# Kernel optimization log

Measured on AMD Instinct MI355X. Metric: run time of the kernel, lower is better.

## Reference

```python
import jax, jax.numpy as jnp
import numpy as np

V, E, H, B, S, SRC, NLEV = 50000, 512, 1024, 64, 32, 256, 5


def setup_inputs() -> dict:
    key = jax.random.key(0)
    ks = jax.random.split(key, 16)
    f = lambda k, sh: jax.random.normal(k, sh, dtype=jnp.float32) * 0.02
    z = lambda n: jnp.zeros((n,), jnp.float32)
    return dict(
        inputs=jax.random.randint(ks[0], (NLEV, B, S), 0, V, dtype=jnp.int32),
        input_lens=jax.random.randint(ks[1], (NLEV, B), 2, S + 1, dtype=jnp.int32),
        contexts=jax.random.normal(ks[2], (B, SRC, H), dtype=jnp.float32),
        emb_W=f(ks[3], (V, E)),
        W_ih0=f(ks[4], (4 * H, E)), W_hh0=f(ks[5], (4 * H, H)), b_ih0=z(4 * H), b_hh0=z(4 * H),
        W_ih1=f(ks[6], (4 * H, H)), W_hh1=f(ks[7], (4 * H, H)), b_ih1=z(4 * H), b_hh1=z(4 * H),
        att_in_W=f(ks[8], (H, H)), att_in_b=z(H),
        att_out_W=f(ks[9], (H, 2 * H)), att_out_b=z(H),
        isl_in_W=f(ks[10], (H, E + H)), isl_in_b=z(H),
        isl_out_W=f(ks[11], (H, H + E)), isl_out_b=z(H),
    )


def _lstm_cell(x, h, c, W_ih, W_hh, b_ih, b_hh):
    # torch.nn.LSTMCell gate order: i, f, g, o
    g = x @ W_ih.T + b_ih + h @ W_hh.T + b_hh
    i, f, gg, o = jnp.split(g, 4, axis=-1)
    c2 = jax.nn.sigmoid(f) * c + jax.nn.sigmoid(i) * jnp.tanh(gg)
    h2 = jax.nn.sigmoid(o) * jnp.tanh(c2)
    return h2, c2


def reference(inputs, input_lens, contexts, emb_W,
              W_ih0, W_hh0, b_ih0, b_hh0, W_ih1, W_hh1, b_ih1, b_hh1,
              att_in_W, att_in_b, att_out_W, att_out_b,
              isl_in_W, isl_in_b, isl_out_W, isl_out_b):
    L, Bb, Ss = inputs.shape
    plevels = inputs[:-1]                       # [L-1, B, S] parent levels
    levels = inputs[1:, :, :-1]                 # [L-1, B, S-1] decoded levels
    plens = input_lens[:-1]                     # [L-1, B]
    # mask[idx][1:l-1] = 1 per original code
    pos = jnp.arange(Ss)
    mask = ((pos[None, None, :] >= 1) & (pos[None, None, :] < (plens[..., None] - 1))).astype(contexts.dtype)
    pembs = emb_W[plevels] * mask[..., None]    # [L-1, B, S, E]
    # init_state: pooled masked parent embeddings + pooled encoder context
    pe = pembs.mean(axis=2)                     # [L-1, B, E]
    cm = jnp.broadcast_to(contexts.mean(axis=1)[None], (L - 1, Bb, contexts.shape[-1]))
    h0 = jnp.tanh(jnp.concatenate([pe, cm], -1) @ isl_in_W.T + isl_in_b)   # [L-1, B, H]
    c0 = jnp.tanh(jnp.concatenate([cm, pe], -1) @ isl_out_W.T + isl_out_b)  # [L-1, B, H]
    h0s = jnp.stack([h0, h0], axis=1)           # [L-1, 2, B, H] same init for both layers
    c0s = jnp.stack([c0, c0], axis=1)

    xs_all = emb_W[levels].transpose(0, 2, 1, 3)  # [L-1, T, B, E]

    def run_level(h0_l, c0_l, xs):
        def step(carry, x):
            h, c = carry                         # [2, B, H] each
            h1, c1 = _lstm_cell(x, h[0], c[0], W_ih0, W_hh0, b_ih0, b_hh0)
            h2, c2 = _lstm_cell(h1, h[1], c[1], W_ih1, W_hh1, b_ih1, b_hh1)
            # global (Luong general) attention
            gamma = h2 @ att_in_W.T + att_in_b   # [B, H]
            w = jax.nn.softmax(jnp.einsum('bsh,bh->bs', contexts, gamma), axis=-1)
            ct = jnp.einsum('bs,bsh->bh', w, contexts)
            out = jnp.tanh(jnp.concatenate([ct, h2], -1) @ att_out_W.T + att_out_b)
            return (jnp.stack([h1, h2]), jnp.stack([c1, c2])), out
        (hT, cT), outs = jax.lax.scan(step, (h0_l, c0_l), xs)
        return outs, hT, cT

    outs, hT, cT = jax.vmap(run_level)(h0s, c0s, xs_all)  # outs: [L-1, T, B, H]
    return outs, hT[-1], cT[-1]
```

## Files before the change

kernel.cpp:

```cpp
#include <hip/hip_runtime.h>
#include <math.h>

#define E 512
#define H 1024
#define B 64
#define S 32
#define SRC 256
#define L4 4
#define T 31
#define R 256

typedef unsigned int uint_t;
typedef unsigned short ushort_t;
typedef float f32x4_v __attribute__((ext_vector_type(4)));
typedef short bf16x8_v __attribute__((ext_vector_type(8)));
typedef _Float16 f16x8_v __attribute__((ext_vector_type(8)));

__device__ __forceinline__ void split1(float x, uint_t& h, uint_t& l) {
    uint_t u = __float_as_uint(x);
    h = u >> 16;
    float hf = __uint_as_float(u & 0xFFFF0000u);
    l = __float_as_uint(x - hf) >> 16;
}

__device__ __forceinline__ void split_quad(float4 v, uint2& hi, uint2& lo) {
    uint_t h0, h1, h2, h3, l0, l1, l2, l3;
    split1(v.x, h0, l0); split1(v.y, h1, l1);
    split1(v.z, h2, l2); split1(v.w, h3, l3);
    hi.x = h0 | (h1 << 16); hi.y = h2 | (h3 << 16);
    lo.x = l0 | (l1 << 16); lo.y = l2 | (l3 << 16);
}

__device__ __forceinline__ ushort_t f16of(float x) {
    _Float16 h = (_Float16)x;
    return *(ushort_t*)&h;
}

__device__ __forceinline__ void splitf16(float x, ushort_t& h, ushort_t& l) {
    _Float16 hh = (_Float16)x;
    float hf = (float)hh;
    _Float16 hl = (_Float16)(x - hf);
    h = *(ushort_t*)&hh;
    l = *(ushort_t*)&hl;
}

__device__ __forceinline__ void gl_lds16(const void* g, void* l) {
    __builtin_amdgcn_global_load_lds(
        (const __attribute__((address_space(1))) void*)g,
        (__attribute__((address_space(3))) void*)l, 16, 0, 0);
}

__global__ __launch_bounds__(128) void k_embed(const int* __restrict__ inputs,
                                               const float* __restrict__ embW,
                                               ushort_t* __restrict__ x16) {
    int blk = blockIdx.x;
    int b = blk % B;
    int t = (blk / B) % T;
    int l = blk / (B * T);
    int tok = inputs[(l + 1) * B * S + b * S + t];
    const float4* src = (const float4*)(embW + (long long)tok * E);
    float4 v = src[threadIdx.x];
    uint_t w0 = f16of(v.x) | ((uint_t)f16of(v.y) << 16);
    uint_t w1 = f16of(v.z) | ((uint_t)f16of(v.w) << 16);
    size_t base = ((size_t)t * R + (size_t)l * B + b) * E + threadIdx.x * 4;
    uint2 pk = {w0, w1};
    *(uint2*)(x16 + base) = pk;
}

__global__ __launch_bounds__(128) void k_pe(const int* __restrict__ inputs,
                                            const int* __restrict__ lens,
                                            const float* __restrict__ embW,
                                            ushort_t* __restrict__ phi,
                                            ushort_t* __restrict__ plo) {
    int r = blockIdx.x;
    int l = r >> 6, b = r & 63;
    int plen = lens[l * B + b];
    int send = plen - 1;
    if (send > S) send = S;
    const int* toks = inputs + l * B * S + b * S;
    float4 acc = {0.f, 0.f, 0.f, 0.f};
    for (int s = 1; s < send; ++s) {
        int tok = toks[s];
        float4 v = ((const float4*)(embW + (long long)tok * E))[threadIdx.x];
        acc.x += v.x; acc.y += v.y; acc.z += v.z; acc.w += v.w;
    }
    const float inv = 1.f / 32.f;
    acc.x *= inv; acc.y *= inv; acc.z *= inv; acc.w *= inv;
    uint2 hi, lo; split_quad(acc, hi, lo);
    size_t base = (size_t)r * E + threadIdx.x * 4;
    *(uint2*)(phi + base) = hi;
    *(uint2*)(plo + base) = lo;
}

__global__ __launch_bounds__(256) void k_cm(const float* __restrict__ ctx,
                                            ushort_t* __restrict__ chi,
                                            ushort_t* __restrict__ clo) {
    int b = blockIdx.x;
    int j = threadIdx.x;
    const float4* c4 = (const float4*)(ctx + (size_t)b * SRC * H);
    float4 acc = {0.f, 0.f, 0.f, 0.f};
    for (int s = 0; s < SRC; ++s) {
        float4 v = c4[(size_t)s * (H / 4) + j];
        acc.x += v.x; acc.y += v.y; acc.z += v.z; acc.w += v.w;
    }
    const float inv = 1.f / (float)SRC;
    acc.x *= inv; acc.y *= inv; acc.z *= inv; acc.w *= inv;
    uint2 hi, lo; split_quad(acc, hi, lo);
    size_t base = (size_t)b * H + j * 4;
    *(uint2*)(chi + base) = hi;
    *(uint2*)(clo + base) = lo;
}

__global__ __launch_bounds__(256) void k_wsplit(
    const float* __restrict__ src1, int ld1, int o1, int Ka,
    const float* __restrict__ src2, int ld2, int o2, int Kb,
    int rowmap, ushort_t* __restrict__ dhi, ushort_t* __restrict__ dlo) {
    int n = blockIdx.x;
    int KT = Ka + Kb;
    long long r = rowmap ? ((long long)(n & 3) * H + (n >> 2)) : (long long)n;
    for (int k4 = threadIdx.x; k4 < (KT >> 2); k4 += 256) {
        int k = k4 << 2;
        float4 v = (k < Ka) ? *(const float4*)(src1 + r * ld1 + o1 + k)
                            : *(const float4*)(src2 + r * ld2 + o2 + (k - Ka));
        uint2 hi, lo; split_quad(v, hi, lo);
        size_t base = (size_t)n * KT + k;
        *(uint2*)(dhi + base) = hi;
        *(uint2*)(dlo + base) = lo;
    }
}

__global__ __launch_bounds__(256) void k_wtile(
    const float* __restrict__ src1, int ld1, int o1, int Ka,
    const float* __restrict__ src2, int ld2, int o2, int Kb,
    int rowmap, unsigned char* __restrict__ panel) {
    int cb = blockIdx.x, t = blockIdx.y;
    int KT = Ka + Kb;
    int NT = KT >> 6;
    size_t obase = ((size_t)cb * NT + t) * 16384;
    int k0 = t << 6;
    for (int q = threadIdx.x; q < 512; q += 256) {
        int s = q >> 6, l = q & 63;
        int n = cb * 64 + 8 * s + (l >> 3);
        long long r = rowmap ? ((long long)(n & 3) * H + (n >> 2)) : (long long)n;
        int xorc = ((l & 7) * 16) ^ ((l >> 3) << 4);
        int ke = k0 + (xorc >> 1);
        const float* sp = (ke < Ka) ? (src1 + r * ld1 + o1 + ke)
                                    : (src2 + r * ld2 + o2 + (ke - Ka));
        float4 v01 = *(const float4*)sp;
        float4 v23 = *(const float4*)(sp + 4);
        uint2 h0, l0, h1, l1;
        split_quad(v01, h0, l0);
        split_quad(v23, h1, l1);
        uint4 hi = {h0.x, h0.y, h1.x, h1.y};
        uint4 lo = {l0.x, l0.y, l1.x, l1.y};
        *(uint4*)(panel + obase + s * 1024 + l * 16) = hi;
        *(uint4*)(panel + obase + 8192 + s * 1024 + l * 16) = lo;
    }
}

__global__ __launch_bounds__(256) void k_wtile16(
    const float* __restrict__ src1, int ld1, int Ka,
    const float* __restrict__ src2, int ld2, int Kb,
    int rowmap, unsigned char* __restrict__ panel) {
    int cb = blockIdx.x, t = blockIdx.y;
    int KT = Ka + Kb;
    int NT = KT >> 6;
    size_t obase = ((size_t)cb * NT + t) * 16384;
    int k0 = t << 6;
    for (int q = threadIdx.x; q < 512; q += 256) {
        int s = q >> 6, l = q & 63;
        int n = cb * 64 + 8 * s + (l >> 3);
        long long r = rowmap ? ((long long)(n & 3) * H + (n >> 2)) : (long long)n;
        int xorc = ((l & 7) * 16) ^ ((l >> 3) << 4);
        int ke = k0 + (xorc >> 1);
        const float* sp = (ke < Ka) ? (src1 + r * ld1 + ke)
                                    : (src2 + r * ld2 + (ke - Ka));
        ushort_t hh[8], ll[8];
#pragma unroll
        for (int e = 0; e < 8; ++e) splitf16(sp[e], hh[e], ll[e]);
        uint4 hi = {(uint_t)hh[0] | ((uint_t)hh[1] << 16),
                    (uint_t)hh[2] | ((uint_t)hh[3] << 16),
                    (uint_t)hh[4] | ((uint_t)hh[5] << 16),
                    (uint_t)hh[6] | ((uint_t)hh[7] << 16)};
        uint4 lo = {(uint_t)ll[0] | ((uint_t)ll[1] << 16),
                    (uint_t)ll[2] | ((uint_t)ll[3] << 16),
                    (uint_t)ll[4] | ((uint_t)ll[5] << 16),
                    (uint_t)ll[6] | ((uint_t)ll[7] << 16)};
        *(uint4*)(panel + obase + s * 1024 + l * 16) = hi;
        *(uint4*)(panel + obase + 8192 + s * 1024 + l * 16) = lo;
    }
}

__global__ __launch_bounds__(256) void k_wtile16s(
    const float* __restrict__ src1, int ld1, int Ka,
    const float* __restrict__ src2, int ld2, int Kb,
    unsigned char* __restrict__ panel) {
    int cb = blockIdx.x, t = blockIdx.y;
    int KT = Ka + Kb;
    int NT = KT >> 6;
    size_t obase = ((size_t)cb * NT + t) * 8192;
    int k0 = t << 6;
    for (int q = threadIdx.x; q < 512; q += 256) {
        int s = q >> 6, l = q & 63;
        int n = cb * 64 + 8 * s + (l >> 3);
        long long r = (long long)(n & 3) * H + (n >> 2);
        int xorc = ((l & 7) * 16) ^ ((l >> 3) << 4);
        int ke = k0 + (xorc >> 1);
        const float* sp = (ke < Ka) ? (src1 + r * ld1 + ke)
                                    : (src2 + r * ld2 + (ke - Ka));
        ushort_t hh[8];
#pragma unroll
        for (int e = 0; e < 8; ++e) hh[e] = f16of(sp[e]);
        uint4 hi = {(uint_t)hh[0] | ((uint_t)hh[1] << 16),
                    (uint_t)hh[2] | ((uint_t)hh[3] << 16),
                    (uint_t)hh[4] | ((uint_t)hh[5] << 16),
                    (uint_t)hh[6] | ((uint_t)hh[7] << 16)};
        *(uint4*)(panel + obase + s * 1024 + l * 16) = hi;
    }
}

__global__ __launch_bounds__(256) void k_wtileT(
    const float* __restrict__ src, int ld, int K,
    unsigned char* __restrict__ panel) {
    int cb = blockIdx.x, t = blockIdx.y;
    int NT = K >> 6;
    size_t obase = ((size_t)cb * NT + t) * 16384;
    int k0 = t << 6;
    for (int q = threadIdx.x; q < 512; q += 256) {
        int s = q >> 6, l = q & 63;
        int n = cb * 64 + 8 * s + (l >> 3);
        int xorc = ((l & 7) * 16) ^ ((l >> 3) << 4);
        int ke = k0 + (xorc >> 1);
        float4 v01, v23;
        v01.x = src[(size_t)(ke + 0) * ld + n];
        v01.y = src[(size_t)(ke + 1) * ld + n];
        v01.z = src[(size_t)(ke + 2) * ld + n];
        v01.w = src[(size_t)(ke + 3) * ld + n];
        v23.x = src[(size_t)(ke + 4) * ld + n];
        v23.y = src[(size_t)(ke + 5) * ld + n];
        v23.z = src[(size_t)(ke + 6) * ld + n];
        v23.w = src[(size_t)(ke + 7) * ld + n];
        uint2 h0, l0, h1, l1;
        split_quad(v01, h0, l0);
        split_quad(v23, h1, l1);
        uint4 hi = {h0.x, h0.y, h1.x, h1.y};
        uint4 lo = {l0.x, l0.y, l1.x, l1.y};
        *(uint4*)(panel + obase + s * 1024 + l * 16) = hi;
        *(uint4*)(panel + obase + 8192 + s * 1024 + l * 16) = lo;
    }
}

__global__ __launch_bounds__(256) void k_g2(
    const ushort_t* __restrict__ Ah1, const ushort_t* __restrict__ Al1, int K1,
    const ushort_t* __restrict__ Ah2, const ushort_t* __restrict__ Al2, int K2,
    int a2mod,
    const unsigned char* __restrict__ Bp,
    const float* __restrict__ bias1, const float* __restrict__ bias2,
    int mode, float* __restrict__ C,
    long long strideT, long long strideL, long long strideB, int act,
    ushort_t* __restrict__ ohi, ushort_t* __restrict__ olo) {
    __shared__ __align__(16) unsigned char lds[65536];
    const int tid = threadIdx.x;
    const int lane = tid & 63;
    const int wv = tid >> 6;
    const int wm = wv & 1, wn = wv >> 1;
    const int cblk = blockIdx.x;
    const int mblk = blockIdx.y;
    const int m0 = mblk * 64;
    const int colbase = cblk * 64;
    const int KT = K1 + K2;
    const int NT = KT >> 6;
    const int n1steps = K1 >> 6;
    const size_t pbase = (size_t)cblk * NT * 16384;

    f32x4_v zero = {0.f, 0.f, 0.f, 0.f};
    f32x4_v acc[2][2] = {{zero, zero}, {zero, zero}};
    const int xorc = ((lane & 7) * 16) ^ ((lane >> 3) << 4);
    const int rsub = lane >> 3;

    auto stage = [&](int t, int buf) {
        unsigned char* dstA = lds + buf * 16384;
        unsigned char* dstB = lds + 32768 + buf * 16384;
        {
            const ushort_t *Ph, *Pl; int lda, k0, mod;
            if (t < n1steps) { Ph = Ah1; Pl = Al1; lda = K1; k0 = t << 6; mod = 0; }
            else { Ph = Ah2; Pl = Al2; lda = K2; k0 = (t - n1steps) << 6; mod = a2mod; }
#pragma unroll
            for (int cc = 0; cc < 4; ++cc) {
                int c = wv * 4 + cc;
                int p = c >> 3, s = c & 7;
                int rr = m0 + 8 * s + rsub;
                if (mod) rr &= (mod - 1);
                const ushort_t* plane = p ? Pl : Ph;
                gl_lds16((const unsigned char*)(plane + (size_t)rr * lda + k0) + xorc,
                         dstA + c * 1024);
            }
        }
        {
            const unsigned char* tb = Bp + pbase + (size_t)t * 16384;
#pragma unroll
            for (int cc = 0; cc < 4; ++cc) {
                int c = wv * 4 + cc;
                gl_lds16(tb + c * 1024 + lane * 16, dstB + c * 1024);
            }
        }
    };
    auto compute = [&](int buf) {
        const unsigned char* Ab = lds + buf * 16384;
        const unsigned char* Bb = lds + 32768 + buf * 16384;
#pragma unroll
        for (int kf = 0; kf < 2; ++kf) {
            int colA = (kf * 64 + ((lane >> 4) * 16)) ^ ((lane & 7) << 4);
            bf16x8_v ah[2], al[2], bh[2], bl[2];
#pragma unroll
            for (int i = 0; i < 2; ++i) {
                int rowm = (wm * 2 + i) * 16 + (lane & 15);
                ah[i] = *(const bf16x8_v*)(Ab + rowm * 128 + colA);
                al[i] = *(const bf16x8_v*)(Ab + 8192 + rowm * 128 + colA);
                int rj = (wn * 2 + i) * 16 + (lane & 15);
                bh[i] = *(const bf16x8_v*)(Bb + rj * 128 + colA);
                bl[i] = *(const bf16x8_v*)(Bb + 8192 + rj * 128 + colA);
            }
            __builtin_amdgcn_s_setprio(1);
#pragma unroll
            for (int i = 0; i < 2; ++i)
#pragma unroll
                for (int j = 0; j < 2; ++j) {
                    acc[i][j] = __builtin_amdgcn_mfma_f32_16x16x32_bf16(al[i], bh[j], acc[i][j], 0, 0, 0);
                    acc[i][j] = __builtin_amdgcn_mfma_f32_16x16x32_bf16(ah[i], bl[j], acc[i][j], 0, 0, 0);
                    acc[i][j] = __builtin_amdgcn_mfma_f32_16x16x32_bf16(ah[i], bh[j], acc[i][j], 0, 0, 0);
                }
            __builtin_amdgcn_s_setprio(0);
        }
    };

    stage(0, 0);
    int cur = 0;
    for (int tt = 0; tt < NT; ++tt) {
        if (tt + 1 < NT) {
            stage(tt + 1, cur ^ 1);
            asm volatile("s_waitcnt vmcnt(8)" ::: "memory");
        } else {
            asm volatile("s_waitcnt vmcnt(0)" ::: "memory");
        }
        __builtin_amdgcn_s_barrier();
        __builtin_amdgcn_sched_barrier(0);
        compute(cur);
        __builtin_amdgcn_sched_barrier(0);
        __builtin_amdgcn_s_barrier();
        cur ^= 1;
    }

    const int l16 = lane & 15, g4 = (lane >> 4) * 4;
#pragma unroll
    for (int i = 0; i < 2; ++i) {
#pragma unroll
        for (int r = 0; r < 4; ++r) {
            int m = m0 + wm * 32 + i * 16 + g4 + r;
            long long rowoff = (long long)(m >> 8) * strideT
                             + (long long)((m >> 6) & 3) * strideL
                             + (long long)(m & 63) * strideB;
#pragma unroll
            for (int jj = 0; jj < 2; ++jj) {
                int n = colbase + wn * 32 + jj * 16 + l16;
                float v = acc[i][jj][r];
                if (mode == 0) {
                    if (bias1) v += bias1[n];
                    if (bias2) v += bias2[n];
                    if (act) v = tanhf(v);
                    C[rowoff + n] = v;
                } else {
                    uint_t hu, lu; split1(v, hu, lu);
                    ohi[rowoff + n] = (ushort_t)hu;
                    olo[rowoff + n] = (ushort_t)lu;
                }
            }
        }
    }
}

__global__ __launch_bounds__(256) void k_g2h(
    const ushort_t* __restrict__ A1, int K1,
    const ushort_t* __restrict__ A2, int K2,
    const unsigned char* __restrict__ Bp,
    const float* __restrict__ bias1,
    float* __restrict__ C,
    long long strideT, long long strideL, long long strideB) {
    __shared__ __align__(16) unsigned char lds[49152];
    const int tid = threadIdx.x;
    const int lane = tid & 63;
    const int wv = tid >> 6;
    const int wm = wv & 1, wn = wv >> 1;
    const int cblk = blockIdx.x;
    const int m0 = blockIdx.y * 64;
    const int colbase = cblk * 64;
    const int KT = K1 + K2;
    const int NT = KT >> 6;
    const int n1steps = K1 >> 6;
    const size_t pbase = (size_t)cblk * NT * 16384;

    f32x4_v zero = {0.f, 0.f, 0.f, 0.f};
    f32x4_v acc[2][2] = {{zero, zero}, {zero, zero}};
    const int xorc = ((lane & 7) * 16) ^ ((lane >> 3) << 4);
    const int rsub = lane >> 3;

    auto stage = [&](int t, int buf) {
        unsigned char* base = lds + buf * 24576;
        const ushort_t* Ap; int lda, k0;
        if (t < n1steps) { Ap = A1; lda = K1; k0 = t << 6; }
        else             { Ap = A2; lda = K2; k0 = (t - n1steps) << 6; }
        const unsigned char* tb = Bp + pbase + (size_t)t * 16384;
#pragma unroll
        for (int cc = 0; cc < 6; ++cc) {
            int c = wv * 6 + cc;
            if (c < 8) {
                int rr = m0 + 8 * c + rsub;
                gl_lds16((const unsigned char*)(Ap + (size_t)rr * lda + k0) + xorc,
                         base + c * 1024);
            } else {
                gl_lds16(tb + (c - 8) * 1024 + lane * 16, base + c * 1024);
            }
        }
    };
    auto compute = [&](int buf) {
        const unsigned char* Ab = lds + buf * 24576;
        const unsigned char* Bb = Ab + 8192;
#pragma unroll
        for (int kf = 0; kf < 2; ++kf) {
            int colA = (kf * 64 + ((lane >> 4) * 16)) ^ ((lane & 7) << 4);
            f16x8_v a[2], bh[2], bl[2];
#pragma unroll
            for (int i = 0; i < 2; ++i) {
                int rowm = (wm * 2 + i) * 16 + (lane & 15);
                a[i] = *(const f16x8_v*)(Ab + rowm * 128 + colA);
                int rj = (wn * 2 + i) * 16 + (lane & 15);
                bh[i] = *(const f16x8_v*)(Bb + rj * 128 + colA);
                bl[i] = *(const f16x8_v*)(Bb + 8192 + rj * 128 + colA);
            }
            __builtin_amdgcn_s_setprio(1);
#pragma unroll
            for (int i = 0; i < 2; ++i)
#pragma unroll
                for (int j = 0; j < 2; ++j) {
                    acc[i][j] = __builtin_amdgcn_mfma_f32_16x16x32_f16(a[i], bl[j], acc[i][j], 0, 0, 0);
                    acc[i][j] = __builtin_amdgcn_mfma_f32_16x16x32_f16(a[i], bh[j], acc[i][j], 0, 0, 0);
                }
            __builtin_amdgcn_s_setprio(0);
        }
    };

    stage(0, 0);
    int cur = 0;
    for (int tt = 0; tt < NT; ++tt) {
        if (tt + 1 < NT) {
            stage(tt + 1, cur ^ 1);
            asm volatile("s_waitcnt vmcnt(6)" ::: "memory");
        } else {
            asm volatile("s_waitcnt vmcnt(0)" ::: "memory");
        }
        __builtin_amdgcn_s_barrier();
        __builtin_amdgcn_sched_barrier(0);
        compute(cur);
        __builtin_amdgcn_sched_barrier(0);
        __builtin_amdgcn_s_barrier();
        cur ^= 1;
    }

    const int l16 = lane & 15, g4 = (lane >> 4) * 4;
#pragma unroll
    for (int i = 0; i < 2; ++i) {
#pragma unroll
        for (int r = 0; r < 4; ++r) {
            int m = m0 + wm * 32 + i * 16 + g4 + r;
            long long rowoff = (long long)(m >> 8) * strideT
                             + (long long)((m >> 6) & 3) * strideL
                             + (long long)(m & 63) * strideB;
#pragma unroll
            for (int jj = 0; jj < 2; ++jj) {
                int n = colbase + wn * 32 + jj * 16 + l16;
                C[rowoff + n] = tanhf(acc[i][jj][r] + bias1[n]);
            }
        }
    }
}

struct GateJob {
    const ushort_t *A1, *A2;
    const unsigned char* Bp;
    const float *bias1, *bias2;
    float *cbuf, *hf;
    ushort_t *h16;
    ushort_t *hhi, *hlo;
    int K1, K2;
};

__global__ __launch_bounds__(256) void k_gatepair(GateJob j0, GateJob j1) {
    __shared__ __align__(16) unsigned char lds[32768];
    const bool sec = blockIdx.y >= 4;
    const ushort_t* A1v = sec ? j1.A1 : j0.A1;
    const ushort_t* A2v = sec ? j1.A2 : j0.A2;
    const unsigned char* Bp = sec ? j1.Bp : j0.Bp;
    const float* bias1  = sec ? j1.bias1 : j0.bias1;
    const float* bias2  = sec ? j1.bias2 : j0.bias2;
    float* cbuf         = sec ? j1.cbuf : j0.cbuf;
    float* hf           = sec ? j1.hf   : j0.hf;
    ushort_t* h16       = sec ? j1.h16  : j0.h16;
    ushort_t* hhi       = sec ? j1.hhi  : j0.hhi;
    ushort_t* hlo       = sec ? j1.hlo  : j0.hlo;
    const int K1        = sec ? j1.K1   : j0.K1;
    const int K2        = sec ? j1.K2   : j0.K2;

    const int tid = threadIdx.x;
    const int lane = tid & 63;
    const int wv = tid >> 6;
    const int wm = wv & 1, wn = wv >> 1;
    const int mblk = blockIdx.y & 3;
    const int cblk = blockIdx.x;
    const int m0 = mblk * 64;
    const int KT = K1 + K2;
    const int NT = KT >> 6;
    const int n1steps = K1 >> 6;
    const size_t pbase = (size_t)cblk * NT * 8192;

    f32x4_v zero = {0.f, 0.f, 0.f, 0.f};
    f32x4_v acc[2][2] = {{zero, zero}, {zero, zero}};
    const int xorc = ((lane & 7) * 16) ^ ((lane >> 3) << 4);
    const int rsub = lane >> 3;

    auto stage = [&](int t, int buf) {
        unsigned char* base = lds + buf * 16384;
        const ushort_t* Ap; int lda, k0;
        if (t < n1steps) { Ap = A1v; lda = K1; k0 = t << 6; }
        else             { Ap = A2v; lda = K2; k0 = (t - n1steps) << 6; }
        const unsigned char* tb = Bp + pbase + (size_t)t * 8192;
#pragma unroll
        for (int cc = 0; cc < 4; ++cc) {
            int c = wv * 4 + cc;
            if (c < 8) {
                int rr = m0 + 8 * c + rsub;
                gl_lds16((const unsigned char*)(Ap + (size_t)rr * lda + k0) + xorc,
                         base + c * 1024);
            } else {
                gl_lds16(tb + (c - 8) * 1024 + lane * 16, base + c * 1024);
            }
        }
    };
    auto compute = [&](int buf) {
        const unsigned char* Ab = lds + buf * 16384;
        const unsigned char* Bb = Ab + 8192;
#pragma unroll
        for (int kf = 0; kf < 2; ++kf) {
            int colA = (kf * 64 + ((lane >> 4) * 16)) ^ ((lane & 7) << 4);
            f16x8_v a[2], bv[2];
#pragma unroll
            for (int i = 0; i < 2; ++i) {
                int rowm = (wm * 2 + i) * 16 + (lane & 15);
                a[i] = *(const f16x8_v*)(Ab + rowm * 128 + colA);
                int rj = (wn * 2 + i) * 16 + (lane & 15);
                bv[i] = *(const f16x8_v*)(Bb + rj * 128 + colA);
            }
            __builtin_amdgcn_s_setprio(1);
#pragma unroll
            for (int i = 0; i < 2; ++i)
#pragma unroll
                for (int j = 0; j < 2; ++j)
                    acc[i][j] = __builtin_amdgcn_mfma_f32_16x16x32_f16(a[i], bv[j], acc[i][j], 0, 0, 0);
            __builtin_amdgcn_s_setprio(0);
        }
    };

    stage(0, 0);
    int cur = 0;
    for (int tt = 0; tt < NT; ++tt) {
        if (tt + 1 < NT) {
            stage(tt + 1, cur ^ 1);
            asm volatile("s_waitcnt vmcnt(4)" ::: "memory");
        } else {
            asm volatile("s_waitcnt vmcnt(0)" ::: "memory");
        }
        __builtin_amdgcn_s_barrier();
        __builtin_amdgcn_sched_barrier(0);
        compute(cur);
        __builtin_amdgcn_sched_barrier(0);
        __builtin_amdgcn_s_barrier();
        cur ^= 1;
    }

    float* gtile = (float*)lds;
    const int l16 = lane & 15, g4 = (lane >> 4) * 4;
#pragma unroll
    for (int i = 0; i < 2; ++i)
#pragma unroll
        for (int jj = 0; jj < 2; ++jj)
#pragma unroll
            for (int r = 0; r < 4; ++r)
                gtile[(wm * 32 + i * 16 + g4 + r) * 68 + wn * 32 + jj * 16 + l16] = acc[i][jj][r];
    __syncthreads();

    int m = tid >> 2;
    int hcb = (tid & 3) * 4;
    int nh0 = cblk * 16;
#pragma unroll
    for (int e = 0; e < 4; ++e) {
        int hc = hcb + e;
        float gv[4];
#pragma unroll
        for (int q = 0; q < 4; ++q) {
            int bidx = q * H + nh0 + hc;
            gv[q] = gtile[m * 68 + hc * 4 + q] + bias1[bidx] + bias2[bidx];
        }
        size_t idx = (size_t)(m0 + m) * H + nh0 + hc;
        float cp = cbuf[idx];
        float si = 1.f / (1.f + __expf(-gv[0]));
        float sf = 1.f / (1.f + __expf(-gv[1]));
        float so = 1.f / (1.f + __expf(-gv[3]));
        float c = sf * cp + si * tanhf(gv[2]);
        float hn = so * tanhf(c);
        cbuf[idx] = c;
        hf[idx] = hn;
        h16[idx] = f16of(hn);
        if (hhi) {
            uint_t hu, lu; split1(hn, hu, lu);
            hhi[idx] = (ushort_t)hu;
            hlo[idx] = (ushort_t)lu;
        }
    }
}

__global__ __launch_bounds__(256) void k_smfma(
    const ushort_t* __restrict__ h1h, const ushort_t* __restrict__ h1l,
    const ushort_t* __restrict__ cwh, const ushort_t* __restrict__ cwl,
    float* __restrict__ scores) {
    __shared__ __align__(16) unsigned char lds[65536];
    const int tid = threadIdx.x;
    const int lane = tid & 63;
    const int wv = tid >> 6;
    const int wm = wv & 1, wn = wv >> 1;
    const int b = blockIdx.z;
    const int m0 = blockIdx.y * 64;
    const int colbase = blockIdx.x * 64;
    const int NT = 16;

    f32x4_v zero = {0.f, 0.f, 0.f, 0.f};
    f32x4_v acc[2][2] = {{zero, zero}, {zero, zero}};
    const int xorc = ((lane & 7) * 16) ^ ((lane >> 3) << 4);
    const int rsub = lane >> 3;

    auto stage = [&](int t, int buf) {
        unsigned char* dstA = lds + buf * 16384;
        unsigned char* dstB = lds + 32768 + buf * 16384;
        int k0 = t << 6;
#pragma unroll
        for (int cc = 0; cc < 4; ++cc) {
            int c = wv * 4 + cc;
            int p = c >> 3, s = c & 7;
            int rr = m0 + 8 * s + rsub;
            int tt = rr >> 2; if (tt > 30) tt = 30;
            size_t row = (size_t)tt * R + (rr & 3) * 64 + b;
            const ushort_t* plane = p ? h1l : h1h;
            gl_lds16((const unsigned char*)(plane + row * H + k0) + xorc,
                     dstA + c * 1024);
        }
#pragma unroll
        for (int cc = 0; cc < 4; ++cc) {
            int c = wv * 4 + cc;
            int p = c >> 3, s = c & 7;
            int rr = colbase + 8 * s + rsub;
            const ushort_t* plane = p ? cwl : cwh;
            gl_lds16((const unsigned char*)(plane + ((size_t)b * SRC + rr) * H + k0) + xorc,
                     dstB + c * 1024);
        }
    };
    auto compute = [&](int buf) {
        const unsigned char* Ab = lds + buf * 16384;
        const unsigned char* Bb = lds + 32768 + buf * 16384;
#pragma unroll
        for (int kf = 0; kf < 2; ++kf) {
            int colA = (kf * 64 + ((lane >> 4) * 16)) ^ ((lane & 7) << 4);
            bf16x8_v ah[2], al[2], bh[2], bl[2];
#pragma unroll
            for (int i = 0; i < 2; ++i) {
                int rowm = (wm * 2 + i) * 16 + (lane & 15);
                ah[i] = *(const bf16x8_v*)(Ab + rowm * 128 + colA);
                al[i] = *(const bf16x8_v*)(Ab + 8192 + rowm * 128 + colA);
                int rj = (wn * 2 + i) * 16 + (lane & 15);
                bh[i] = *(const bf16x8_v*)(Bb + rj * 128 + colA);
                bl[i] = *(const bf16x8_v*)(Bb + 8192 + rj * 128 + colA);
            }
            __builtin_amdgcn_s_setprio(1);
#pragma unroll
            for (int i = 0; i < 2; ++i)
#pragma unroll
                for (int j = 0; j < 2; ++j) {
                    acc[i][j] = __builtin_amdgcn_mfma_f32_16x16x32_bf16(al[i], bh[j], acc[i][j], 0, 0, 0);
                    acc[i][j] = __builtin_amdgcn_mfma_f32_16x16x32_bf16(ah[i], bl[j], acc[i][j], 0, 0, 0);
                    acc[i][j] = __builtin_amdgcn_mfma_f32_16x16x32_bf16(ah[i], bh[j], acc[i][j], 0, 0, 0);
                }
            __builtin_amdgcn_s_setprio(0);
        }
    };

    stage(0, 0);
    int cur = 0;
    for (int tt = 0; tt < NT; ++tt) {
        if (tt + 1 < NT) {
            stage(tt + 1, cur ^ 1);
            asm volatile("s_waitcnt vmcnt(8)" ::: "memory");
        } else {
            asm volatile("s_waitcnt vmcnt(0)" ::: "memory");
        }
        __builtin_amdgcn_s_barrier();
        __builtin_amdgcn_sched_barrier(0);
        compute(cur);
        __builtin_amdgcn_sched_barrier(0);
        __builtin_amdgcn_s_barrier();
        cur ^= 1;
    }

    const int l16 = lane & 15, g4 = (lane >> 4) * 4;
#pragma unroll
    for (int i = 0; i < 2; ++i) {
#pragma unroll
        for (int jj = 0; jj < 2; ++jj) {
#pragma unroll
            for (int r = 0; r < 4; ++r) {
                int m = m0 + wm * 32 + i * 16 + g4 + r;
                int t = m >> 2;
                if (t < 31) {
                    size_t row = (size_t)t * R + (m & 3) * 64 + b;
                    int n = colbase + wn * 32 + jj * 16 + l16;
                    scores[row * SRC + n] = acc[i][jj][r];
                }
            }
        }
    }
}

__global__ __launch_bounds__(256) void k_smax(const float* __restrict__ scores,
                                              const float* __restrict__ cb,
                                              float* __restrict__ w) {
    int t = blockIdx.x, b = blockIdx.y;
    int l = threadIdx.x >> 6, lane = threadIdx.x & 63;
    size_t row = (size_t)t * R + l * 64 + b;
    const float* sr = scores + row * SRC;
    const float* cbb = cb + b * SRC;
    float v0 = sr[lane] + cbb[lane];
    float v1 = sr[lane + 64] + cbb[lane + 64];
    float v2 = sr[lane + 128] + cbb[lane + 128];
    float v3 = sr[lane + 192] + cbb[lane + 192];
    float m = fmaxf(fmaxf(v0, v1), fmaxf(v2, v3));
#pragma unroll
    for (int off = 32; off >= 1; off >>= 1) m = fmaxf(m, __shfl_xor(m, off));
    float e0 = expf(v0 - m), e1 = expf(v1 - m), e2 = expf(v2 - m), e3 = expf(v3 - m);
    float sum = e0 + e1 + e2 + e3;
#pragma unroll
    for (int off = 32; off >= 1; off >>= 1) sum += __shfl_xor(sum, off);
    float inv = 1.f / sum;
    float* wr = w + row * SRC;
    wr[lane] = e0 * inv;
    wr[lane + 64] = e1 * inv;
    wr[lane + 128] = e2 * inv;
    wr[lane + 192] = e3 * inv;
}

__global__ __launch_bounds__(512) void k_ct_all(const float* __restrict__ ctx,
                                                const float* __restrict__ w,
                                                ushort_t* __restrict__ ct16) {
    __shared__ float ws[32][260];
    const int b = blockIdx.x, tc = blockIdx.y;
    const int tid = threadIdx.x;
    for (int q = tid; q < 32 * 64; q += 512) {
        int r = q >> 6, c4 = q & 63;
        int t = tc * 8 + (r >> 2);
        float4 v = {0.f, 0.f, 0.f, 0.f};
        if (t < 31)
            v = *(const float4*)(w + ((size_t)t * R + (r & 3) * 64 + b) * SRC + c4 * 4);
        *(float4*)&ws[r][c4 * 4] = v;
    }
    __syncthreads();

    float2 acc[32];
#pragma unroll
    for (int r = 0; r < 32; ++r) acc[r] = make_float2(0.f, 0.f);
    const float2* base = (const float2*)(ctx + (size_t)b * SRC * H) + tid;
    for (int s = 0; s < SRC; s += 4) {
        float2 c0 = base[(size_t)s * (H / 2)];
        float2 c1 = base[(size_t)(s + 1) * (H / 2)];
        float2 c2 = base[(size_t)(s + 2) * (H / 2)];
        float2 c3 = base[(size_t)(s + 3) * (H / 2)];
#pragma unroll
        for (int r = 0; r < 32; ++r) {
            float4 wv = *(const float4*)&ws[r][s];
            acc[r].x += wv.x * c0.x + wv.y * c1.x + wv.z * c2.x + wv.w * c3.x;
            acc[r].y += wv.x * c0.y + wv.y * c1.y + wv.z * c2.y + wv.w * c3.y;
        }
    }
#pragma unroll
    for (int r = 0; r < 32; ++r) {
        int t = tc * 8 + (r >> 2);
        if (t < 31) {
            size_t obase = ((size_t)t * R + (r & 3) * 64 + b) * H + tid * 2;
            uint_t pk = f16of(acc[r].x) | ((uint_t)f16of(acc[r].y) << 16);
            *(uint_t*)(ct16 + obase) = pk;
        }
    }
}

__global__ __launch_bounds__(256) void k_init_split(const float* __restrict__ h0f,
                                                    const float* __restrict__ c0f,
                                                    float* __restrict__ h1f,
                                                    float* __restrict__ c1f,
                                                    ushort_t* __restrict__ h0_16,
                                                    ushort_t* __restrict__ h1i_16) {
    int idx = blockIdx.x * 256 + threadIdx.x;
    float h = h0f[idx], c = c0f[idx];
    h1f[idx] = h; c1f[idx] = c;
    ushort_t hv = f16of(h);
    h0_16[idx] = hv;
    h1i_16[idx] = hv;
}

__global__ __launch_bounds__(256) void k_cb(const float* __restrict__ ctx,
                                            const float* __restrict__ bvec,
                                            float* __restrict__ cb) {
    int b = blockIdx.x, ch = blockIdx.y;
    int wave = threadIdx.x >> 6, lane = threadIdx.x & 63;
    for (int i = 0; i < 16; ++i) {
        int s = ch * 64 + wave * 16 + i;
        const float* cs = ctx + ((size_t)b * SRC + s) * H;
        float a = 0.f;
#pragma unroll
        for (int j = 0; j < 4; ++j) {
            float4 cv = *(const float4*)(cs + lane * 4 + j * 256);
            float4 bv = *(const float4*)(bvec + lane * 4 + j * 256);
            a += cv.x * bv.x + cv.y * bv.y + cv.z * bv.z + cv.w * bv.w;
        }
#pragma unroll
        for (int off = 32; off >= 1; off >>= 1) a += __shfl_xor(a, off);
        if (lane == 0) cb[b * SRC + s] = a;
    }
}

extern "C" void kernel_launch(void* const* d_in, const int* in_sizes, int n_in,
                              void* d_out, int out_size, void* d_ws, size_t ws_size,
                              hipStream_t stream) {
    const int*   inputs     = (const int*)d_in[0];
    const int*   input_lens = (const int*)d_in[1];
    const float* contexts   = (const float*)d_in[2];
    const float* emb_W      = (const float*)d_in[3];
    const float* W_ih0      = (const float*)d_in[4];
    const float* W_hh0      = (const float*)d_in[5];
    const float* b_ih0      = (const float*)d_in[6];
    const float* b_hh0      = (const float*)d_in[7];
    const float* W_ih1      = (const float*)d_in[8];
    const float* W_hh1      = (const float*)d_in[9];
    const float* b_ih1      = (const float*)d_in[10];
    const float* b_hh1      = (const float*)d_in[11];
    const float* att_in_W   = (const float*)d_in[12];
    const float* att_in_b   = (const float*)d_in[13];
    const float* att_out_W  = (const float*)d_in[14];
    const float* att_out_b  = (const float*)d_in[15];
    const float* isl_in_W   = (const float*)d_in[16];
    const float* isl_in_b   = (const float*)d_in[17];
    const float* isl_out_W  = (const float*)d_in[18];
    const float* isl_out_b  = (const float*)d_in[19];

    float* out = (float*)d_out;

    char* p = (char*)d_ws;
    auto alloc = [&](size_t bytes) { char* r = p; p += (bytes + 255) & ~(size_t)255; return r; };
    ushort_t* xs16 = (ushort_t*)alloc((size_t)T * R * E * 2);
    ushort_t* h016[2];
    h016[0] = (ushort_t*)alloc((size_t)R * H * 2);
    h016[1] = (ushort_t*)alloc((size_t)R * H * 2);
    ushort_t* h1i16 = (ushort_t*)alloc((size_t)R * H * 2);
    ushort_t* h116all = (ushort_t*)alloc((size_t)T * R * H * 2);
    ushort_t* h1hall = (ushort_t*)alloc((size_t)T * R * H * 2);
    ushort_t* h1lall = (ushort_t*)alloc((size_t)T * R * H * 2);
    ushort_t* pehi = (ushort_t*)alloc((size_t)R * E * 2);
    ushort_t* pelo = (ushort_t*)alloc((size_t)R * E * 2);
    ushort_t* cmhi = (ushort_t*)alloc((size_t)B * H * 2);
    ushort_t* cmlo = (ushort_t*)alloc((size_t)B * H * 2);
    unsigned char* wg0p = (unsigned char*)alloc((size_t)64 * 24 * 8192);
    unsigned char* wg1p = (unsigned char*)alloc((size_t)64 * 32 * 8192);
    unsigned char* wgTp = (unsigned char*)alloc((size_t)16 * 16 * 16384);
    unsigned char* wotp = (unsigned char*)alloc((size_t)16 * 32 * 16384);
    unsigned char* wiip = (unsigned char*)alloc((size_t)16 * 24 * 16384);
    unsigned char* wiop = (unsigned char*)alloc((size_t)16 * 24 * 16384);
    ushort_t* cxh = (ushort_t*)alloc((size_t)B * SRC * H * 2);
    ushort_t* cxl = (ushort_t*)alloc((size_t)B * SRC * H * 2);
    ushort_t* cwh = (ushort_t*)alloc((size_t)B * SRC * H * 2);
    ushort_t* cwl = (ushort_t*)alloc((size_t)B * SRC * H * 2);
    float* cbv = (float*)alloc((size_t)B * SRC * 4);
    float* h0f = (float*)alloc((size_t)R * H * 4);
    float* h1f = (float*)alloc((size_t)R * H * 4);
    float* c0f = (float*)alloc((size_t)R * H * 4);
    float* c1f = (float*)alloc((size_t)R * H * 4);
    float* scores = (float*)cxh;
    float* wbuf   = scores + (size_t)T * R * SRC;
    ushort_t* ct16 = (ushort_t*)(wbuf + (size_t)T * R * SRC);

    k_embed<<<L4 * T * B, 128, 0, stream>>>(inputs, emb_W, xs16);
    k_pe<<<R, 128, 0, stream>>>(inputs, input_lens, emb_W, pehi, pelo);
    k_cm<<<B, 256, 0, stream>>>(contexts, cmhi, cmlo);
    k_wtile16s<<<dim3(64, 24), 256, 0, stream>>>(W_ih0, 512, 512, W_hh0, 1024, 1024, wg0p);
    k_wtile16s<<<dim3(64, 32), 256, 0, stream>>>(W_ih1, 1024, 1024, W_hh1, 1024, 1024, wg1p);
    k_wtile16<<<dim3(16, 32), 256, 0, stream>>>(att_out_W, 2048, 2048, nullptr, 0, 0, 0, wotp);
    k_wtileT<<<dim3(16, 16), 256, 0, stream>>>(att_in_W, 1024, 1024, wgTp);
    k_wtile<<<dim3(16, 24), 256, 0, stream>>>(isl_in_W, 1536, 0, 1536, nullptr, 0, 0, 0, 0, wiip);
    k_wtile<<<dim3(16, 24), 256, 0, stream>>>(isl_out_W, 1536, 1024, 512, isl_out_W, 1536, 0, 1024, 0, wiop);
    k_wsplit<<<B * SRC, 256, 0, stream>>>(contexts, 1024, 0, 1024, nullptr, 0, 0, 0, 0, cxh, cxl);

    k_g2<<<dim3(16, 4), 256, 0, stream>>>(pehi, pelo, 512, cmhi, cmlo, 1024, 64,
                                          wiip, isl_in_b, nullptr, 0,
                                          h0f, 0, 64LL * H, (long long)H, 1,
                                          nullptr, nullptr);
    k_g2<<<dim3(16, 4), 256, 0, stream>>>(pehi, pelo, 512, cmhi, cmlo, 1024, 64,
                                          wiop, isl_out_b, nullptr, 0,
                                          c0f, 0, 64LL * H, (long long)H, 1,
                                          nullptr, nullptr);
    k_init_split<<<R * H / 256, 256, 0, stream>>>(h0f, c0f, h1f, c1f, h016[0], h1i16);

    k_g2<<<dim3(16, 256), 256, 0, stream>>>(cxh, cxl, 1024,
                                            nullptr, nullptr, 0, 0,
                                            wgTp, nullptr, nullptr, 2,
                                            nullptr, (long long)SRC * H, 64LL * H, (long long)H, 0,
                                            cwh, cwl);
    k_cb<<<dim3(B, 4), 256, 0, stream>>>(contexts, att_in_b, cbv);

    int cur = 0;
    for (int L = 0; L <= T; ++L) {
        bool has0 = (L < T), has1 = (L > 0);
        GateJob g0 = {}, g1 = {};
        if (has0) {
            g0.A1 = xs16 + (size_t)L * R * E;
            g0.A2 = h016[cur];
            g0.Bp = wg0p;
            g0.bias1 = b_ih0;  g0.bias2 = b_hh0;
            g0.cbuf = c0f;  g0.hf = h0f;
            g0.h16 = h016[cur ^ 1];
            g0.hhi = nullptr;  g0.hlo = nullptr;
            g0.K1 = E;  g0.K2 = H;
        }
        if (has1) {
            g1.A1 = h016[cur];
            g1.A2 = (L == 1) ? h1i16 : h116all + (size_t)(L - 2) * R * H;
            g1.Bp = wg1p;
            g1.bias1 = b_ih1;  g1.bias2 = b_hh1;
            g1.cbuf = c1f;  g1.hf = h1f;
            g1.h16 = h116all + (size_t)(L - 1) * R * H;
            g1.hhi = h1hall + (size_t)(L - 1) * R * H;
            g1.hlo = h1lall + (size_t)(L - 1) * R * H;
            g1.K1 = H;  g1.K2 = H;
        }
        if (has0 && has1)
            k_gatepair<<<dim3(64, 8), 256, 0, stream>>>(g0, g1);
        else if (has0)
            k_gatepair<<<dim3(64, 4), 256, 0, stream>>>(g0, g0);
        else
            k_gatepair<<<dim3(64, 4), 256, 0, stream>>>(g1, g1);
        if (has0) cur ^= 1;
    }

    k_smfma<<<dim3(4, 2, B), 256, 0, stream>>>(h1hall, h1lall, cwh, cwl, scores);
    k_smax<<<dim3(T, B), 256, 0, stream>>>(scores, cbv, wbuf);
    k_ct_all<<<dim3(B, 4), 512, 0, stream>>>(contexts, wbuf, ct16);
    k_g2h<<<dim3(16, 124), 256, 0, stream>>>(ct16, 1024, h116all, 1024,
                                             wotp, att_out_b,
                                             out, (long long)B * H,
                                             (long long)T * B * H, (long long)H);

    size_t OUTS = (size_t)L4 * T * B * H;
    size_t seg = (size_t)B * H;
    hipMemcpyAsync(out + OUTS,           h0f + 192 * H, seg * 4, hipMemcpyDeviceToDevice, stream);
    hipMemcpyAsync(out + OUTS + seg,     h1f + 192 * H, seg * 4, hipMemcpyDeviceToDevice, stream);
    hipMemcpyAsync(out + OUTS + 2 * seg, c0f + 192 * H, seg * 4, hipMemcpyDeviceToDevice, stream);
    hipMemcpyAsync(out + OUTS + 3 * seg, c1f + 192 * H, seg * 4, hipMemcpyDeviceToDevice, stream);
}
```

Measured before the change: 1.256 ms.

## Compute attention gamma per step instead of projecting contexts; deepen gate pipeline

The old path projected every context row through att_in_W (a 16K-row GEMM) and added a separate bias-score kernel. The new path applies att_in_W to the decoded h2 states instead, producing gamma in hi/lo split form, and scores gamma against the raw split contexts. This removes the large context projection, the bias dot-product kernel and the hi/lo split writes inside the recurrent gate kernel. Separately, the gate kernel's K-loop goes from double buffering to a 4-stage LDS pipeline with 64KB of shared memory, which may reduce occupancy.

```diff
diff --git a/kernel.cpp b/kernel.cpp
--- a/kernel.cpp
+++ b/kernel.cpp
@@ -219,37 +219,6 @@
     }
 }
 
-__global__ __launch_bounds__(256) void k_wtileT(
-    const float* __restrict__ src, int ld, int K,
-    unsigned char* __restrict__ panel) {
-    int cb = blockIdx.x, t = blockIdx.y;
-    int NT = K >> 6;
-    size_t obase = ((size_t)cb * NT + t) * 16384;
-    int k0 = t << 6;
-    for (int q = threadIdx.x; q < 512; q += 256) {
-        int s = q >> 6, l = q & 63;
-        int n = cb * 64 + 8 * s + (l >> 3);
-        int xorc = ((l & 7) * 16) ^ ((l >> 3) << 4);
-        int ke = k0 + (xorc >> 1);
-        float4 v01, v23;
-        v01.x = src[(size_t)(ke + 0) * ld + n];
-        v01.y = src[(size_t)(ke + 1) * ld + n];
-        v01.z = src[(size_t)(ke + 2) * ld + n];
-        v01.w = src[(size_t)(ke + 3) * ld + n];
-        v23.x = src[(size_t)(ke + 4) * ld + n];
-        v23.y = src[(size_t)(ke + 5) * ld + n];
-        v23.z = src[(size_t)(ke + 6) * ld + n];
-        v23.w = src[(size_t)(ke + 7) * ld + n];
-        uint2 h0, l0, h1, l1;
-        split_quad(v01, h0, l0);
-        split_quad(v23, h1, l1);
-        uint4 hi = {h0.x, h0.y, h1.x, h1.y};
-        uint4 lo = {l0.x, l0.y, l1.x, l1.y};
-        *(uint4*)(panel + obase + s * 1024 + l * 16) = hi;
-        *(uint4*)(panel + obase + 8192 + s * 1024 + l * 16) = lo;
-    }
-}
-
 __global__ __launch_bounds__(256) void k_g2(
     const ushort_t* __restrict__ Ah1, const ushort_t* __restrict__ Al1, int K1,
     const ushort_t* __restrict__ Ah2, const ushort_t* __restrict__ Al2, int K2,
@@ -384,8 +353,9 @@
     const ushort_t* __restrict__ A2, int K2,
     const unsigned char* __restrict__ Bp,
     const float* __restrict__ bias1,
-    float* __restrict__ C,
-    long long strideT, long long strideL, long long strideB) {
+    int mode, float* __restrict__ C,
+    long long strideT, long long strideL, long long strideB,
+    ushort_t* __restrict__ ohi, ushort_t* __restrict__ olo) {
     __shared__ __align__(16) unsigned char lds[49152];
     const int tid = threadIdx.x;
     const int lane = tid & 63;
@@ -478,7 +448,14 @@
 #pragma unroll
             for (int jj = 0; jj < 2; ++jj) {
                 int n = colbase + wn * 32 + jj * 16 + l16;
-                C[rowoff + n] = tanhf(acc[i][jj][r] + bias1[n]);
+                float v = acc[i][jj][r] + bias1[n];
+                if (mode == 0) {
+                    C[rowoff + n] = tanhf(v);
+                } else {
+                    uint_t hu, lu; split1(v, hu, lu);
+                    ohi[rowoff + n] = (ushort_t)hu;
+                    olo[rowoff + n] = (ushort_t)lu;
+                }
             }
         }
     }
@@ -490,12 +467,11 @@
     const float *bias1, *bias2;
     float *cbuf, *hf;
     ushort_t *h16;
-    ushort_t *hhi, *hlo;
     int K1, K2;
 };
 
 __global__ __launch_bounds__(256) void k_gatepair(GateJob j0, GateJob j1) {
-    __shared__ __align__(16) unsigned char lds[32768];
+    __shared__ __align__(16) unsigned char lds[65536];
     const bool sec = blockIdx.y >= 4;
     const ushort_t* A1v = sec ? j1.A1 : j0.A1;
     const ushort_t* A2v = sec ? j1.A2 : j0.A2;
@@ -505,8 +481,6 @@
     float* cbuf         = sec ? j1.cbuf : j0.cbuf;
     float* hf           = sec ? j1.hf   : j0.hf;
     ushort_t* h16       = sec ? j1.h16  : j0.h16;
-    ushort_t* hhi       = sec ? j1.hhi  : j0.hhi;
-    ushort_t* hlo       = sec ? j1.hlo  : j0.hlo;
     const int K1        = sec ? j1.K1   : j0.K1;
     const int K2        = sec ? j1.K2   : j0.K2;
 
@@ -570,20 +544,24 @@
     };
 
     stage(0, 0);
-    int cur = 0;
+    stage(1, 1);
+    stage(2, 2);
     for (int tt = 0; tt < NT; ++tt) {
-        if (tt + 1 < NT) {
-            stage(tt + 1, cur ^ 1);
+        if (tt + 3 < NT) {
+            stage(tt + 3, (tt + 3) & 3);
+            asm volatile("s_waitcnt vmcnt(12)" ::: "memory");
+        } else if (tt + 2 < NT) {
+            asm volatile("s_waitcnt vmcnt(8)" ::: "memory");
+        } else if (tt + 1 < NT) {
             asm volatile("s_waitcnt vmcnt(4)" ::: "memory");
         } else {
             asm volatile("s_waitcnt vmcnt(0)" ::: "memory");
         }
         __builtin_amdgcn_s_barrier();
         __builtin_amdgcn_sched_barrier(0);
-        compute(cur);
+        compute(tt & 3);
         __builtin_amdgcn_sched_barrier(0);
         __builtin_amdgcn_s_barrier();
-        cur ^= 1;
     }
 
     float* gtile = (float*)lds;
@@ -619,17 +597,12 @@
         cbuf[idx] = c;
         hf[idx] = hn;
         h16[idx] = f16of(hn);
-        if (hhi) {
-            uint_t hu, lu; split1(hn, hu, lu);
-            hhi[idx] = (ushort_t)hu;
-            hlo[idx] = (ushort_t)lu;
-        }
     }
 }
 
 __global__ __launch_bounds__(256) void k_smfma(
-    const ushort_t* __restrict__ h1h, const ushort_t* __restrict__ h1l,
-    const ushort_t* __restrict__ cwh, const ushort_t* __restrict__ cwl,
+    const ushort_t* __restrict__ gah, const ushort_t* __restrict__ gal,
+    const ushort_t* __restrict__ cxh, const ushort_t* __restrict__ cxl,
     float* __restrict__ scores) {
     __shared__ __align__(16) unsigned char lds[65536];
     const int tid = threadIdx.x;
@@ -657,7 +630,7 @@
             int rr = m0 + 8 * s + rsub;
             int tt = rr >> 2; if (tt > 30) tt = 30;
             size_t row = (size_t)tt * R + (rr & 3) * 64 + b;
-            const ushort_t* plane = p ? h1l : h1h;
+            const ushort_t* plane = p ? gal : gah;
             gl_lds16((const unsigned char*)(plane + row * H + k0) + xorc,
                      dstA + c * 1024);
         }
@@ -666,7 +639,7 @@
             int c = wv * 4 + cc;
             int p = c >> 3, s = c & 7;
             int rr = colbase + 8 * s + rsub;
-            const ushort_t* plane = p ? cwl : cwh;
+            const ushort_t* plane = p ? cxl : cxh;
             gl_lds16((const unsigned char*)(plane + ((size_t)b * SRC + rr) * H + k0) + xorc,
                      dstB + c * 1024);
         }
@@ -737,17 +710,15 @@
 }
 
 __global__ __launch_bounds__(256) void k_smax(const float* __restrict__ scores,
-                                              const float* __restrict__ cb,
                                               float* __restrict__ w) {
     int t = blockIdx.x, b = blockIdx.y;
     int l = threadIdx.x >> 6, lane = threadIdx.x & 63;
     size_t row = (size_t)t * R + l * 64 + b;
     const float* sr = scores + row * SRC;
-    const float* cbb = cb + b * SRC;
-    float v0 = sr[lane] + cbb[lane];
-    float v1 = sr[lane + 64] + cbb[lane + 64];
-    float v2 = sr[lane + 128] + cbb[lane + 128];
-    float v3 = sr[lane + 192] + cbb[lane + 192];
+    float v0 = sr[lane];
+    float v1 = sr[lane + 64];
+    float v2 = sr[lane + 128];
+    float v3 = sr[lane + 192];
     float m = fmaxf(fmaxf(v0, v1), fmaxf(v2, v3));
 #pragma unroll
     for (int off = 32; off >= 1; off >>= 1) m = fmaxf(m, __shfl_xor(m, off));
@@ -818,27 +789,6 @@
     ushort_t hv = f16of(h);
     h0_16[idx] = hv;
     h1i_16[idx] = hv;
-}
-
-__global__ __launch_bounds__(256) void k_cb(const float* __restrict__ ctx,
-                                            const float* __restrict__ bvec,
-                                            float* __restrict__ cb) {
-    int b = blockIdx.x, ch = blockIdx.y;
-    int wave = threadIdx.x >> 6, lane = threadIdx.x & 63;
-    for (int i = 0; i < 16; ++i) {
-        int s = ch * 64 + wave * 16 + i;
-        const float* cs = ctx + ((size_t)b * SRC + s) * H;
-        float a = 0.f;
-#pragma unroll
-        for (int j = 0; j < 4; ++j) {
-            float4 cv = *(const float4*)(cs + lane * 4 + j * 256);
-            float4 bv = *(const float4*)(bvec + lane * 4 + j * 256);
-            a += cv.x * bv.x + cv.y * bv.y + cv.z * bv.z + cv.w * bv.w;
-        }
-#pragma unroll
-        for (int off = 32; off >= 1; off >>= 1) a += __shfl_xor(a, off);
-        if (lane == 0) cb[b * SRC + s] = a;
-    }
 }
 
 extern "C" void kernel_launch(void* const* d_in, const int* in_sizes, int n_in,
@@ -875,38 +825,35 @@
     h016[1] = (ushort_t*)alloc((size_t)R * H * 2);
     ushort_t* h1i16 = (ushort_t*)alloc((size_t)R * H * 2);
     ushort_t* h116all = (ushort_t*)alloc((size_t)T * R * H * 2);
-    ushort_t* h1hall = (ushort_t*)alloc((size_t)T * R * H * 2);
-    ushort_t* h1lall = (ushort_t*)alloc((size_t)T * R * H * 2);
+    ushort_t* gamh = (ushort_t*)alloc((size_t)T * R * H * 2);
+    ushort_t* gaml = (ushort_t*)alloc((size_t)T * R * H * 2);
     ushort_t* pehi = (ushort_t*)alloc((size_t)R * E * 2);
     ushort_t* pelo = (ushort_t*)alloc((size_t)R * E * 2);
     ushort_t* cmhi = (ushort_t*)alloc((size_t)B * H * 2);
     ushort_t* cmlo = (ushort_t*)alloc((size_t)B * H * 2);
     unsigned char* wg0p = (unsigned char*)alloc((size_t)64 * 24 * 8192);
     unsigned char* wg1p = (unsigned char*)alloc((size_t)64 * 32 * 8192);
-    unsigned char* wgTp = (unsigned char*)alloc((size_t)16 * 16 * 16384);
+    unsigned char* wgip = (unsigned char*)alloc((size_t)16 * 16 * 16384);
     unsigned char* wotp = (unsigned char*)alloc((size_t)16 * 32 * 16384);
     unsigned char* wiip = (unsigned char*)alloc((size_t)16 * 24 * 16384);
     unsigned char* wiop = (unsigned char*)alloc((size_t)16 * 24 * 16384);
     ushort_t* cxh = (ushort_t*)alloc((size_t)B * SRC * H * 2);
     ushort_t* cxl = (ushort_t*)alloc((size_t)B * SRC * H * 2);
-    ushort_t* cwh = (ushort_t*)alloc((size_t)B * SRC * H * 2);
-    ushort_t* cwl = (ushort_t*)alloc((size_t)B * SRC * H * 2);
-    float* cbv = (float*)alloc((size_t)B * SRC * 4);
     float* h0f = (float*)alloc((size_t)R * H * 4);
     float* h1f = (float*)alloc((size_t)R * H * 4);
     float* c0f = (float*)alloc((size_t)R * H * 4);
     float* c1f = (float*)alloc((size_t)R * H * 4);
-    float* scores = (float*)cxh;
-    float* wbuf   = scores + (size_t)T * R * SRC;
-    ushort_t* ct16 = (ushort_t*)(wbuf + (size_t)T * R * SRC);
+    float* scores = (float*)alloc((size_t)T * R * SRC * 4);
+    float* wbuf   = (float*)alloc((size_t)T * R * SRC * 4);
+    ushort_t* ct16 = (ushort_t*)alloc((size_t)T * R * H * 2);
 
     k_embed<<<L4 * T * B, 128, 0, stream>>>(inputs, emb_W, xs16);
     k_pe<<<R, 128, 0, stream>>>(inputs, input_lens, emb_W, pehi, pelo);
     k_cm<<<B, 256, 0, stream>>>(contexts, cmhi, cmlo);
     k_wtile16s<<<dim3(64, 24), 256, 0, stream>>>(W_ih0, 512, 512, W_hh0, 1024, 1024, wg0p);
     k_wtile16s<<<dim3(64, 32), 256, 0, stream>>>(W_ih1, 1024, 1024, W_hh1, 1024, 1024, wg1p);
+    k_wtile16<<<dim3(16, 16), 256, 0, stream>>>(att_in_W, 1024, 1024, nullptr, 0, 0, 0, wgip);
     k_wtile16<<<dim3(16, 32), 256, 0, stream>>>(att_out_W, 2048, 2048, nullptr, 0, 0, 0, wotp);
-    k_wtileT<<<dim3(16, 16), 256, 0, stream>>>(att_in_W, 1024, 1024, wgTp);
     k_wtile<<<dim3(16, 24), 256, 0, stream>>>(isl_in_W, 1536, 0, 1536, nullptr, 0, 0, 0, 0, wiip);
     k_wtile<<<dim3(16, 24), 256, 0, stream>>>(isl_out_W, 1536, 1024, 512, isl_out_W, 1536, 0, 1024, 0, wiop);
     k_wsplit<<<B * SRC, 256, 0, stream>>>(contexts, 1024, 0, 1024, nullptr, 0, 0, 0, 0, cxh, cxl);
@@ -920,13 +867,6 @@
                                           c0f, 0, 64LL * H, (long long)H, 1,
                                           nullptr, nullptr);
     k_init_split<<<R * H / 256, 256, 0, stream>>>(h0f, c0f, h1f, c1f, h016[0], h1i16);
-
-    k_g2<<<dim3(16, 256), 256, 0, stream>>>(cxh, cxl, 1024,
-                                            nullptr, nullptr, 0, 0,
-                                            wgTp, nullptr, nullptr, 2,
-                                            nullptr, (long long)SRC * H, 64LL * H, (long long)H, 0,
-                                            cwh, cwl);
-    k_cb<<<dim3(B, 4), 256, 0, stream>>>(contexts, att_in_b, cbv);
 
     int cur = 0;
     for (int L = 0; L <= T; ++L) {
@@ -939,7 +879,6 @@
             g0.bias1 = b_ih0;  g0.bias2 = b_hh0;
             g0.cbuf = c0f;  g0.hf = h0f;
             g0.h16 = h016[cur ^ 1];
-            g0.hhi = nullptr;  g0.hlo = nullptr;
             g0.K1 = E;  g0.K2 = H;
         }
         if (has1) {
@@ -949,8 +888,6 @@
             g1.bias1 = b_ih1;  g1.bias2 = b_hh1;
             g1.cbuf = c1f;  g1.hf = h1f;
             g1.h16 = h116all + (size_t)(L - 1) * R * H;
-            g1.hhi = h1hall + (size_t)(L - 1) * R * H;
-            g1.hlo = h1lall + (size_t)(L - 1) * R * H;
             g1.K1 = H;  g1.K2 = H;
         }
         if (has0 && has1)
@@ -962,13 +899,18 @@
         if (has0) cur ^= 1;
     }
 
-    k_smfma<<<dim3(4, 2, B), 256, 0, stream>>>(h1hall, h1lall, cwh, cwl, scores);
-    k_smax<<<dim3(T, B), 256, 0, stream>>>(scores, cbv, wbuf);
+    k_g2h<<<dim3(16, 124), 256, 0, stream>>>(h116all, 1024, h116all, 0,
+                                             wgip, att_in_b, 2,
+                                             nullptr, 256LL * H, 64LL * H, (long long)H,
+                                             gamh, gaml);
+    k_smfma<<<dim3(4, 2, B), 256, 0, stream>>>(gamh, gaml, cxh, cxl, scores);
+    k_smax<<<dim3(T, B), 256, 0, stream>>>(scores, wbuf);
     k_ct_all<<<dim3(B, 4), 512, 0, stream>>>(contexts, wbuf, ct16);
     k_g2h<<<dim3(16, 124), 256, 0, stream>>>(ct16, 1024, h116all, 1024,
-                                             wotp, att_out_b,
+                                             wotp, att_out_b, 0,
                                              out, (long long)B * H,
-                                             (long long)T * B * H, (long long)H);
+                                             (long long)T * B * H, (long long)H,
+                                             nullptr, nullptr);
 
     size_t OUTS = (size_t)L4 * T * B * H;
     size_t seg = (size_t)B * H;
```

New measurement: 1.152 ms. 8.2% less time.
